# Kernel tuning notes

Measured on AMD Instinct MI355X. Metric: run time of the kernel, lower is better.

Reference implementation:

```python
import jax, jax.numpy as jnp
import numpy as np

N = 65536   # mini-batch of per-element losses
C = 1000    # number of classes (logit dim == super-class id range == weight matrix dims)


def setup_inputs() -> dict:
    key = jax.random.key(0)
    k0, k1, k2, k3 = jax.random.split(key, 4)
    logits = jax.random.normal(k0, (N, C), dtype=jnp.float32)
    target = jax.random.randint(k1, (N,), 0, C, dtype=jnp.int64)
    class_weights = jax.random.uniform(k2, (C, C), dtype=jnp.float32)
    super_classes = jax.random.randint(k3, (C,), 0, C, dtype=jnp.int64)
    return {"logits": logits, "class_weights": class_weights,
            "target": target, "super_classes": super_classes}


def reference(logits, class_weights, target, super_classes):
    # log_softmax over class dim (single stable pass)
    logp = jax.nn.log_softmax(logits, axis=1)                      # [N, C]
    # truetarget = super_classes[target]  (super-class id per sample)
    truetarget = super_classes[target]                             # [N]
    # predicted class per sample
    predtarget = jnp.argmax(logp, axis=1)                          # [N]
    # w2 = class_weights[truetarget].gather(1, predtarget) == class_weights[truetarget, predtarget]
    w = class_weights[truetarget, predtarget]                      # [N]
    # logp.index_select(-1, truetarget).diag() == logp[i, truetarget[i]] — direct gather,
    # no O(N^2) intermediate
    tgt_logp = jnp.take_along_axis(logp, truetarget[:, None], axis=1)[:, 0]  # [N]
    l2 = -w * tgt_logp
    l3 = jnp.sum(l2) / jnp.sum(w)
    return l3
```

## Files before the change

kernel.cpp:

```cpp
#include <hip/hip_runtime.h>
#include <math.h>

#define CCOLS 1000
#define NF4   250

__global__ __launch_bounds__(256) void cacel_rows_kernel(
    const float* __restrict__ logits,
    const float* __restrict__ cw,
    const int*   __restrict__ tgt,
    const int*   __restrict__ sc,
    float*       __restrict__ partials,
    int nrows)
{
    const int wid  = threadIdx.x >> 6;
    const int lane = threadIdx.x & 63;
    const int row  = blockIdx.x * 4 + wid;

    float num = 0.0f, den = 0.0f;

    if (row < nrows) {
        const int tt = sc[tgt[row]];

        const float4* rp = (const float4*)(logits + (size_t)row * CCOLS);

        float4 v[4];
#pragma unroll
        for (int it = 0; it < 4; ++it) {
            const int f = it * 64 + lane;
            if (f < NF4) {
                v[it] = rp[f];
            } else {
                v[it] = make_float4(-INFINITY, -INFINITY, -INFINITY, -INFINITY);
            }
        }

        float m  = -INFINITY;
        int   mi = 0x7fffffff;
        float tval = 0.0f;
#pragma unroll
        for (int it = 0; it < 4; ++it) {
            const int cbase = (it * 64 + lane) * 4;
            const float* pv = (const float*)&v[it];
#pragma unroll
            for (int j = 0; j < 4; ++j) {
                const float x = pv[j];
                const int   c = cbase + j;
                if (x > m) { m = x; mi = c; }
                if (c == tt) tval = x;
            }
        }

#pragma unroll
        for (int s = 32; s >= 1; s >>= 1) {
            const float om = __shfl_xor(m,  s, 64);
            const int   oi = __shfl_xor(mi, s, 64);
            if (om > m || (om == m && oi < mi)) { m = om; mi = oi; }
        }

        float ssum = 0.0f;
#pragma unroll
        for (int it = 0; it < 4; ++it) {
            const float* pv = (const float*)&v[it];
#pragma unroll
            for (int j = 0; j < 4; ++j) {
                ssum += __expf(pv[j] - m);
            }
        }
#pragma unroll
        for (int s = 32; s >= 1; s >>= 1) ssum += __shfl_xor(ssum, s, 64);

#pragma unroll
        for (int s = 32; s >= 1; s >>= 1) tval += __shfl_xor(tval, s, 64);

        if (lane == 0) {
            const float lse   = m + __logf(ssum);
            const float tlogp = tval - lse;
            const float w     = cw[(size_t)tt * CCOLS + mi];
            num = -w * tlogp;
            den = w;
        }
    }

    __shared__ float snum[4], sden[4];
    if (lane == 0) { snum[wid] = num; sden[wid] = den; }
    __syncthreads();
    if (threadIdx.x == 0) {
        partials[2 * (size_t)blockIdx.x + 0] = snum[0] + snum[1] + snum[2] + snum[3];
        partials[2 * (size_t)blockIdx.x + 1] = sden[0] + sden[1] + sden[2] + sden[3];
    }
}

__global__ __launch_bounds__(256) void cacel_final_kernel(
    const float* __restrict__ partials, int nblk, float* __restrict__ out)
{
    float n = 0.0f, d = 0.0f;
    for (int i = threadIdx.x; i < nblk; i += 256) {
        n += partials[2 * (size_t)i + 0];
        d += partials[2 * (size_t)i + 1];
    }
    __shared__ float sn[256], sd[256];
    sn[threadIdx.x] = n;
    sd[threadIdx.x] = d;
    __syncthreads();
    for (int s = 128; s > 0; s >>= 1) {
        if (threadIdx.x < s) {
            sn[threadIdx.x] += sn[threadIdx.x + s];
            sd[threadIdx.x] += sd[threadIdx.x + s];
        }
        __syncthreads();
    }
    if (threadIdx.x == 0) out[0] = sn[0] / sd[0];
}

extern "C" void kernel_launch(void* const* d_in, const int* in_sizes, int n_in,
                              void* d_out, int out_size, void* d_ws, size_t ws_size,
                              hipStream_t stream) {
    (void)n_in; (void)out_size; (void)ws_size;
    const float* logits = (const float*)d_in[0];
    const float* cw     = (const float*)d_in[1];
    const int*   tgt    = (const int*)d_in[2];
    const int*   sc     = (const int*)d_in[3];

    const int N    = in_sizes[2];
    const int nblk = (N + 3) / 4;

    float* partials = (float*)d_ws;

    cacel_rows_kernel<<<nblk, 256, 0, stream>>>(logits, cw, tgt, sc, partials, N);
    cacel_final_kernel<<<1, 256, 0, stream>>>(partials, nblk, (float*)d_out);
}
```

Measured before the change: 61.86 us.

## Process eight rows per wave with double-buffered nontemporal row loads

```diff
diff --git a/kernel.cpp b/kernel.cpp
--- a/kernel.cpp
+++ b/kernel.cpp
@@ -3,6 +3,66 @@
 
 #define CCOLS 1000
 #define NF4   250
+#define RPW   8
+#define WPB   4
+
+typedef float f32x4 __attribute__((ext_vector_type(4)));
+
+__device__ __forceinline__ f32x4 ntload(const f32x4* p) {
+    return __builtin_nontemporal_load(p);
+}
+
+__device__ __forceinline__ void loadrow(f32x4& b0, f32x4& b1, f32x4& b2, f32x4& b3,
+                                        const float* __restrict__ logits, int row, int lane) {
+    const f32x4* rp = (const f32x4*)(logits + (size_t)row * CCOLS);
+    b0 = ntload(rp + lane);
+    b1 = ntload(rp + 64 + lane);
+    b2 = ntload(rp + 128 + lane);
+    if (lane < NF4 - 192) {
+        b3 = ntload(rp + 192 + lane);
+    } else {
+        const f32x4 ninf = {-INFINITY, -INFINITY, -INFINITY, -INFINITY};
+        b3 = ninf;
+    }
+}
+
+__device__ __forceinline__ void process_row(f32x4 v0, f32x4 v1, f32x4 v2, f32x4 v3,
+                                            int lane, int tt, float tval,
+                                            const float* __restrict__ cw,
+                                            float& num, float& den) {
+    float m = -INFINITY;
+#pragma unroll
+    for (int j = 0; j < 4; ++j) {
+        m = fmaxf(m, v0[j]); m = fmaxf(m, v1[j]);
+        m = fmaxf(m, v2[j]); m = fmaxf(m, v3[j]);
+    }
+#pragma unroll
+    for (int s = 32; s >= 1; s >>= 1) m = fmaxf(m, __shfl_xor(m, s, 64));
+
+    float ssum = 0.0f;
+    int   mi   = 0x7fffffff;
+#pragma unroll
+    for (int j = 0; j < 4; ++j) {
+        { const float x = v0[j]; const int c = lane * 4 + j;
+          ssum += __expf(x - m); if (x == m) mi = min(mi, c); }
+        { const float x = v1[j]; const int c = (64 + lane) * 4 + j;
+          ssum += __expf(x - m); if (x == m) mi = min(mi, c); }
+        { const float x = v2[j]; const int c = (128 + lane) * 4 + j;
+          ssum += __expf(x - m); if (x == m) mi = min(mi, c); }
+        { const float x = v3[j]; const int c = (192 + lane) * 4 + j;
+          ssum += __expf(x - m); if (x == m) mi = min(mi, c); }
+    }
+#pragma unroll
+    for (int s = 32; s >= 1; s >>= 1) {
+        ssum += __shfl_xor(ssum, s, 64);
+        mi = min(mi, __shfl_xor(mi, s, 64));
+    }
+
+    const float lse = m + __logf(ssum);
+    const float w = cw[(size_t)tt * CCOLS + mi];
+    num += w * (lse - tval);
+    den += w;
+}
 
 __global__ __launch_bounds__(256) void cacel_rows_kernel(
     const float* __restrict__ logits,
@@ -14,74 +74,44 @@
 {
     const int wid  = threadIdx.x >> 6;
     const int lane = threadIdx.x & 63;
-    const int row  = blockIdx.x * 4 + wid;
+    const int W    = blockIdx.x * WPB + wid;
+    const int r0   = __builtin_amdgcn_readfirstlane(W * RPW);
+
+    int   tts[RPW];
+    float tvals[RPW];
+#pragma unroll
+    for (int k = 0; k < RPW; ++k) {
+        const int row = r0 + k;
+        tts[k] = (row < nrows) ? sc[tgt[row]] : 0;
+    }
+#pragma unroll
+    for (int k = 0; k < RPW; ++k) {
+        const int row = r0 + k;
+        tvals[k] = (row < nrows) ? logits[(size_t)row * CCOLS + tts[k]] : 0.0f;
+    }
 
     float num = 0.0f, den = 0.0f;
 
-    if (row < nrows) {
-        const int tt = sc[tgt[row]];
-
-        const float4* rp = (const float4*)(logits + (size_t)row * CCOLS);
-
-        float4 v[4];
-#pragma unroll
-        for (int it = 0; it < 4; ++it) {
-            const int f = it * 64 + lane;
-            if (f < NF4) {
-                v[it] = rp[f];
-            } else {
-                v[it] = make_float4(-INFINITY, -INFINITY, -INFINITY, -INFINITY);
-            }
-        }
-
-        float m  = -INFINITY;
-        int   mi = 0x7fffffff;
-        float tval = 0.0f;
-#pragma unroll
-        for (int it = 0; it < 4; ++it) {
-            const int cbase = (it * 64 + lane) * 4;
-            const float* pv = (const float*)&v[it];
-#pragma unroll
-            for (int j = 0; j < 4; ++j) {
-                const float x = pv[j];
-                const int   c = cbase + j;
-                if (x > m) { m = x; mi = c; }
-                if (c == tt) tval = x;
-            }
-        }
+    f32x4 a0, a1, a2, a3, b0, b1, b2, b3;
+    if (r0 < nrows) loadrow(a0, a1, a2, a3, logits, r0, lane);
 
 #pragma unroll
-        for (int s = 32; s >= 1; s >>= 1) {
-            const float om = __shfl_xor(m,  s, 64);
-            const int   oi = __shfl_xor(mi, s, 64);
-            if (om > m || (om == m && oi < mi)) { m = om; mi = oi; }
-        }
-
-        float ssum = 0.0f;
-#pragma unroll
-        for (int it = 0; it < 4; ++it) {
-            const float* pv = (const float*)&v[it];
-#pragma unroll
-            for (int j = 0; j < 4; ++j) {
-                ssum += __expf(pv[j] - m);
+    for (int k = 0; k < RPW; ++k) {
+        const int row = r0 + k;
+        if (row < nrows) {
+            if ((k & 1) == 0) {
+                if (k + 1 < RPW && row + 1 < nrows)
+                    loadrow(b0, b1, b2, b3, logits, row + 1, lane);
+                process_row(a0, a1, a2, a3, lane, tts[k], tvals[k], cw, num, den);
+            } else {
+                if (k + 1 < RPW && row + 1 < nrows)
+                    loadrow(a0, a1, a2, a3, logits, row + 1, lane);
+                process_row(b0, b1, b2, b3, lane, tts[k], tvals[k], cw, num, den);
             }
-        }
-#pragma unroll
-        for (int s = 32; s >= 1; s >>= 1) ssum += __shfl_xor(ssum, s, 64);
-
-#pragma unroll
-        for (int s = 32; s >= 1; s >>= 1) tval += __shfl_xor(tval, s, 64);
-
-        if (lane == 0) {
-            const float lse   = m + __logf(ssum);
-            const float tlogp = tval - lse;
-            const float w     = cw[(size_t)tt * CCOLS + mi];
-            num = -w * tlogp;
-            den = w;
         }
     }
 
-    __shared__ float snum[4], sden[4];
+    __shared__ float snum[WPB], sden[WPB];
     if (lane == 0) { snum[wid] = num; sden[wid] = den; }
     __syncthreads();
     if (threadIdx.x == 0) {
@@ -122,7 +152,8 @@
     const int*   sc     = (const int*)d_in[3];
 
     const int N    = in_sizes[2];
-    const int nblk = (N + 3) / 4;
+    const int rows_per_block = WPB * RPW;
+    const int nblk = (N + rows_per_block - 1) / rows_per_block;
 
     float* partials = (float*)d_ws;
 
```

Measured after the change: 56.66 us. -8.4%, faster.
